# Kernel optimization log

Measured on AMD Instinct MI355X. Metric: run time of the kernel, lower is better.

## Reference

```python
import jax, jax.numpy as jnp
import numpy as np

N_NODES = 10000
N_EDGES = 80000
A, C, D = 2, 15, 64     # batch, temporal dim (15 fixed by fc conv kernel), feature dim
OUT_DIM = 10            # fixed by fc conv kernel width
N_GIN = 2               # num_layers - 1 GIN conv layers
BN_EPS = 1e-5


def bn_last(x, g, b):
    # torch BatchNorm2d (training-mode batch stats) with channels on the LAST axis;
    # original code permutes (0,3,2,1) around BN, which is equivalent to normalizing axis -1.
    m = x.mean(axis=(0, 1, 2), keepdims=True)
    v = x.var(axis=(0, 1, 2), keepdims=True)  # biased var, as torch uses in forward
    return (x - m) * jax.lax.rsqrt(v + BN_EPS) * g + b


def setup_inputs() -> dict:
    key = jax.random.key(0)
    ks = jax.random.split(key, 16)
    s = 0.05
    f32 = jnp.float32
    return {
        "h": jax.random.normal(ks[0], (A, D, C, N_NODES), f32),
        # GIN layer params, stacked over the 2 layers (input_dim == hidden_dim == 64)
        "eps": jnp.zeros((N_GIN,), f32),                                   # learn_eps, init 0
        "W0": (jax.random.normal(ks[1], (N_GIN, D, D), f32) * s),          # MLP linear 0
        "b0": jnp.zeros((N_GIN, D), f32),
        "g0": jnp.ones((N_GIN, D), f32),                                   # MLP BN
        "be0": jnp.zeros((N_GIN, D), f32),
        "W1": (jax.random.normal(ks[2], (N_GIN, D, D), f32) * s),          # MLP linear 1
        "b1": jnp.zeros((N_GIN, D), f32),
        "ga": jnp.ones((N_GIN, D), f32),                                   # ApplyNodeFunc BN
        "ba": jnp.zeros((N_GIN, D), f32),
        "go": jnp.ones((N_GIN, D), f32),                                   # outer GIN BN
        "bo": jnp.zeros((N_GIN, D), f32),
        # per-hidden-rep prediction linears (3 = num_layers)
        "Wp": (jax.random.normal(ks[3], (N_GIN + 1, D, OUT_DIM), f32) * s),
        "bp": jnp.zeros((N_GIN + 1, OUT_DIM), f32),
        # final Conv2d(1,1,(15,10)) == full-extent weighted sum
        "Wfc": (jax.random.normal(ks[4], (C, OUT_DIM), f32) * s),
        "bfc": jnp.zeros((1,), f32),
        # graph edge list (src -> dst aggregation)
        "src": jax.random.randint(ks[5], (N_EDGES,), 0, N_NODES, jnp.int32),
        "dst": jax.random.randint(ks[6], (N_EDGES,), 0, N_NODES, jnp.int32),
    }


def reference(h, eps, W0, b0, g0, be0, W1, b1, ga, ba, go, bo, Wp, bp, Wfc, bfc, src, dst):
    # h: [A, D, C, N] -> node-first layout [N, A, C, D] (the two transposes in torch)
    x = jnp.transpose(h, (3, 0, 2, 1))
    hidden_rep = [x]
    for l in range(N_GIN):
        # GINConv, sum aggregation: (1+eps)*h + sum_{src->dst} h[src]
        agg = jax.ops.segment_sum(x[src], dst, num_segments=N_NODES)
        z = (1.0 + eps[l]) * x + agg
        # MLP (2 layers): linear -> BN -> relu -> linear
        z = jax.nn.relu(bn_last(z @ W0[l] + b0[l], g0[l], be0[l]))
        z = z @ W1[l] + b1[l]
        # ApplyNodeFunc: BN + relu
        z = jax.nn.relu(bn_last(z, ga[l], ba[l]))
        # outer per-layer BN + relu (GIN.forward)
        x = jax.nn.relu(bn_last(z, go[l], bo[l]))
        hidden_rep.append(x)
    # multi-scale readout: sum-pool over nodes, per-layer linear score (dropout is eval/no-op)
    score = jnp.zeros((A, C, OUT_DIM), h.dtype)
    for i, r in enumerate(hidden_rep):
        pooled = r.sum(axis=0)                       # [A, C, D]
        score = score + pooled @ Wp[i] + bp[i]
    # fc: Conv2d(1,1,(15,10)) over [A,1,C,OUT_DIM] then squeeze twice -> [A, 1]
    out = jnp.einsum('ach,ch->a', score, Wfc) + bfc[0]
    return out[:, None]
```

## Files before the change

### kernel.cpp

```cpp
#include <hip/hip_runtime.h>
#include <hip/hip_bf16.h>

#define N_NODES   10000
#define N_EDGES   80000
#define R_TOTAL   300000
#define ELEMS     19200000
#define NODE_F    1920
#define N_TILES   18750
#define PD_GRID   640
#define GEMM_GRID 1024
#define RP_BGRP   16

typedef __attribute__((ext_vector_type(8))) short short8;
typedef __attribute__((ext_vector_type(4))) float f32x4;
typedef __attribute__((ext_vector_type(4))) unsigned int u32x4;
typedef __attribute__((ext_vector_type(2))) unsigned int u32x2;
typedef unsigned short ushort_t;

__device__ __forceinline__ unsigned short f2bf(float f) {
    unsigned u = __builtin_bit_cast(unsigned, f);
    unsigned r = u + 0x7fff + ((u >> 16) & 1);
    return (unsigned short)(r >> 16);
}
__device__ __forceinline__ float lo_f(unsigned u) { return __builtin_bit_cast(float, u << 16); }
__device__ __forceinline__ float hi_f(unsigned u) { return __builtin_bit_cast(float, u & 0xffff0000u); }
__device__ __forceinline__ unsigned packbf(float lo, float hi) {
    return ((unsigned)f2bf(hi) << 16) | (unsigned)f2bf(lo);
}

__device__ __forceinline__ void bn_coef(const float* __restrict__ ssum,
                                        const float* __restrict__ ssq,
                                        const float* __restrict__ g,
                                        const float* __restrict__ b, int j,
                                        float& sc, float& sh) {
    const float invM = 1.0f / (float)R_TOTAL;
    float m = ssum[j] * invM;
    float v = ssq[j] * invM - m * m;
    sc = g[j] * rsqrtf(v + 1e-5f);
    sh = b[j] - m * sc;
}

__global__ __launch_bounds__(256) void k_transpose(const float* __restrict__ h,
                                                   ushort_t* __restrict__ xb,
                                                   float* __restrict__ pooled) {
    __shared__ float tile[64][65];
    int tn = blockIdx.x;
    int ac = blockIdx.y;
    int a = ac / 15, c = ac % 15;
    int t = threadIdx.x;
    int n0 = tn * 64;

    int r = t >> 4, g = t & 15;
    int nbase = n0 + 4 * g;
    const float* hp = h + (size_t)a * 9600000 + (size_t)c * 10000;
#pragma unroll
    for (int it = 0; it < 4; it++) {
        int d = it * 16 + r;
        const float* p = hp + (size_t)d * 150000 + nbase;
        float4 v;
        if (nbase + 3 < N_NODES) {
            v = *(const float4*)p;
        } else {
            v.x = (nbase + 0 < N_NODES) ? p[0] : 0.f;
            v.y = (nbase + 1 < N_NODES) ? p[1] : 0.f;
            v.z = (nbase + 2 < N_NODES) ? p[2] : 0.f;
            v.w = (nbase + 3 < N_NODES) ? p[3] : 0.f;
        }
        tile[d][4 * g + 0] = v.x;
        tile[d][4 * g + 1] = v.y;
        tile[d][4 * g + 2] = v.z;
        tile[d][4 * g + 3] = v.w;
    }
    __syncthreads();

    int nn = t >> 2, dg = (t & 3) * 16;
    int n = n0 + nn;
    if (n < N_NODES) {
        u32x4 oA, oB;
#pragma unroll
        for (int q = 0; q < 4; q++) {
            oA[q] = packbf(tile[dg + 2 * q][nn],     tile[dg + 2 * q + 1][nn]);
            oB[q] = packbf(tile[dg + 8 + 2 * q][nn], tile[dg + 8 + 2 * q + 1][nn]);
        }
        ushort_t* dst = xb + ((size_t)(n * 30 + ac)) * 64 + dg;
        *(u32x4*)dst = oA;
        *(u32x4*)(dst + 8) = oB;
    }

    if (t < 64) {
        float s = 0.f;
        int lim = min(64, N_NODES - n0);
        for (int j = 0; j < lim; j++) s += tile[t][j];
        atomicAdd(&pooled[ac * 64 + t], s);
    }
}

__global__ void k_deg(const int* __restrict__ dst, int* __restrict__ deg) {
    int e = blockIdx.x * 256 + threadIdx.x;
    if (e < N_EDGES) atomicAdd(&deg[dst[e]], 1);
}

__global__ __launch_bounds__(256) void k_scan(const int* __restrict__ deg,
                                              int* __restrict__ off,
                                              int* __restrict__ cursor) {
    __shared__ int buf[256];
    int t = threadIdx.x;
    int c0 = t * 40;
    int local[40];
    int s = 0;
    for (int i = 0; i < 40; i++) {
        int idx = c0 + i;
        int d = (idx < N_NODES) ? deg[idx] : 0;
        local[i] = d;
        s += d;
    }
    buf[t] = s;
    __syncthreads();
    for (int st = 1; st < 256; st <<= 1) {
        int v = (t >= st) ? buf[t - st] : 0;
        __syncthreads();
        buf[t] += v;
        __syncthreads();
    }
    int run = buf[t] - s;
    for (int i = 0; i < 40; i++) {
        int idx = c0 + i;
        if (idx < N_NODES) {
            off[idx] = run;
            cursor[idx] = run;
            run += local[i];
        }
    }
    if (t == 255) off[N_NODES] = buf[255];
}

__global__ void k_fill(const int* __restrict__ src, const int* __restrict__ dst,
                       int* __restrict__ cursor, int* __restrict__ csr) {
    int e = blockIdx.x * 256 + threadIdx.x;
    if (e < N_EDGES) {
        int p = atomicAdd(&cursor[dst[e]], 1);
        csr[p] = src[e];
    }
}

__global__ __launch_bounds__(256) void k_gather(const ushort_t* __restrict__ xb,
                                                ushort_t* __restrict__ aggb,
                                                const int* __restrict__ off,
                                                const int* __restrict__ csr) {
    __shared__ int eds[256];
    int n = blockIdx.x;
    int t = threadIdx.x;
    bool act = t < 240;
    int e0 = off[n], e1 = off[n + 1];
    float acc[8] = {0.f, 0.f, 0.f, 0.f, 0.f, 0.f, 0.f, 0.f};
    for (int base = e0; base < e1; base += 256) {
        int cnt = min(256, e1 - base);
        __syncthreads();
        if (t < cnt) eds[t] = csr[base + t];
        __syncthreads();
        if (act) {
            int i = 0;
            for (; i + 4 <= cnt; i += 4) {
                u32x4 v0 = *(const u32x4*)(xb + (size_t)eds[i + 0] * NODE_F + t * 8);
                u32x4 v1 = *(const u32x4*)(xb + (size_t)eds[i + 1] * NODE_F + t * 8);
                u32x4 v2 = *(const u32x4*)(xb + (size_t)eds[i + 2] * NODE_F + t * 8);
                u32x4 v3 = *(const u32x4*)(xb + (size_t)eds[i + 3] * NODE_F + t * 8);
#pragma unroll
                for (int q = 0; q < 4; q++) {
                    acc[2 * q]     += lo_f(v0[q]) + lo_f(v1[q]) + lo_f(v2[q]) + lo_f(v3[q]);
                    acc[2 * q + 1] += hi_f(v0[q]) + hi_f(v1[q]) + hi_f(v2[q]) + hi_f(v3[q]);
                }
            }
            for (; i < cnt; i++) {
                u32x4 v = *(const u32x4*)(xb + (size_t)eds[i] * NODE_F + t * 8);
#pragma unroll
                for (int q = 0; q < 4; q++) {
                    acc[2 * q]     += lo_f(v[q]);
                    acc[2 * q + 1] += hi_f(v[q]);
                }
            }
        }
    }
    if (act) {
        u32x4 o;
#pragma unroll
        for (int q = 0; q < 4; q++) o[q] = packbf(acc[2 * q], acc[2 * q + 1]);
        *(u32x4*)(aggb + (size_t)n * NODE_F + t * 8) = o;
    }
}

__global__ __launch_bounds__(256) void k_passA(const ushort_t* __restrict__ xb,
                                               const ushort_t* __restrict__ aggb,
                                               ushort_t* __restrict__ to,
                                               const float* __restrict__ W,
                                               const float* __restrict__ bias,
                                               const float* __restrict__ epsp, int l,
                                               float* __restrict__ ssum, float* __restrict__ ssq) {
    int tid = threadIdx.x;
    int lane = tid & 63, wid = tid >> 6;
    int m = lane & 15, kg = lane >> 4;

    short8 bfr[2][4];
#pragma unroll
    for (int s = 0; s < 2; s++)
#pragma unroll
        for (int nt = 0; nt < 4; nt++) {
            short8 v;
#pragma unroll
            for (int j = 0; j < 8; j++)
                v[j] = (short)f2bf(W[(s * 32 + kg * 8 + j) * 64 + 4 * m + nt]);
            bfr[s][nt] = v;
        }
    float bcol[4];
#pragma unroll
    for (int nt = 0; nt < 4; nt++) bcol[nt] = bias[4 * m + nt];
    float e1 = 1.0f + epsp[l];

    float s0a[4] = {0.f, 0.f, 0.f, 0.f}, s1a[4] = {0.f, 0.f, 0.f, 0.f};

    for (int tile = blockIdx.x * 4 + wid; tile < N_TILES; tile += gridDim.x * 4) {
        size_t row0 = (size_t)tile * 16;
        const u32x4* xr = (const u32x4*)(xb + (row0 + m) * 64);
        const u32x4* ar = (const u32x4*)(aggb + (row0 + m) * 64);
        short8 afr[2];
#pragma unroll
        for (int s = 0; s < 2; s++) {
            u32x4 xv = xr[s * 4 + kg];
            u32x4 av = ar[s * 4 + kg];
            u32x4 zv;
#pragma unroll
            for (int q = 0; q < 4; q++) {
                float zl = fmaf(e1, lo_f(xv[q]), lo_f(av[q]));
                float zh = fmaf(e1, hi_f(xv[q]), hi_f(av[q]));
                zv[q] = packbf(zl, zh);
            }
            afr[s] = __builtin_bit_cast(short8, zv);
        }
        f32x4 acc0 = {0,0,0,0}, acc1 = {0,0,0,0}, acc2 = {0,0,0,0}, acc3 = {0,0,0,0};
#pragma unroll
        for (int s = 0; s < 2; s++) {
            acc0 = __builtin_amdgcn_mfma_f32_16x16x32_bf16(afr[s], bfr[s][0], acc0, 0, 0, 0);
            acc1 = __builtin_amdgcn_mfma_f32_16x16x32_bf16(afr[s], bfr[s][1], acc1, 0, 0, 0);
            acc2 = __builtin_amdgcn_mfma_f32_16x16x32_bf16(afr[s], bfr[s][2], acc2, 0, 0, 0);
            acc3 = __builtin_amdgcn_mfma_f32_16x16x32_bf16(afr[s], bfr[s][3], acc3, 0, 0, 0);
        }
        ushort_t* tw = to + (row0 + kg * 4) * 64 + 4 * m;
#pragma unroll
        for (int r = 0; r < 4; r++) {
            float v0 = acc0[r] + bcol[0];
            float v1 = acc1[r] + bcol[1];
            float v2 = acc2[r] + bcol[2];
            float v3 = acc3[r] + bcol[3];
            u32x2 pk;
            pk[0] = packbf(v0, v1);
            pk[1] = packbf(v2, v3);
            *(u32x2*)(tw + (size_t)r * 64) = pk;
            s0a[0] += v0; s1a[0] += v0 * v0;
            s0a[1] += v1; s1a[1] += v1 * v1;
            s0a[2] += v2; s1a[2] += v2 * v2;
            s0a[3] += v3; s1a[3] += v3 * v3;
        }
    }
    __shared__ float shs0[64], shs1[64];
    if (tid < 64) { shs0[tid] = 0.f; shs1[tid] = 0.f; }
    __syncthreads();
#pragma unroll
    for (int nt = 0; nt < 4; nt++) {
        atomicAdd(&shs0[4 * m + nt], s0a[nt]);
        atomicAdd(&shs1[4 * m + nt], s1a[nt]);
    }
    __syncthreads();
    if (tid < 64) {
        atomicAdd(&ssum[tid], shs0[tid]);
        atomicAdd(&ssq[tid], shs1[tid]);
    }
}

__global__ __launch_bounds__(256) void k_passB(const ushort_t* __restrict__ ti,
                                               ushort_t* __restrict__ to,
                                               const float* __restrict__ W,
                                               const float* __restrict__ bias,
                                               const float* __restrict__ ssum0,
                                               const float* __restrict__ ssq0,
                                               const float* __restrict__ g0,
                                               const float* __restrict__ be0,
                                               float* __restrict__ ssum, float* __restrict__ ssq) {
    int tid = threadIdx.x;
    int lane = tid & 63, wid = tid >> 6;
    int m = lane & 15, kg = lane >> 4;

    short8 bfr[2][4];
#pragma unroll
    for (int s = 0; s < 2; s++)
#pragma unroll
        for (int nt = 0; nt < 4; nt++) {
            short8 v;
#pragma unroll
            for (int j = 0; j < 8; j++)
                v[j] = (short)f2bf(W[(s * 32 + kg * 8 + j) * 64 + 4 * m + nt]);
            bfr[s][nt] = v;
        }
    float bcol[4];
#pragma unroll
    for (int nt = 0; nt < 4; nt++) bcol[nt] = bias[4 * m + nt];
    float scv[2][8], shv[2][8];
#pragma unroll
    for (int s = 0; s < 2; s++)
#pragma unroll
        for (int j = 0; j < 8; j++)
            bn_coef(ssum0, ssq0, g0, be0, s * 32 + kg * 8 + j, scv[s][j], shv[s][j]);

    float s0a[4] = {0.f, 0.f, 0.f, 0.f}, s1a[4] = {0.f, 0.f, 0.f, 0.f};

    for (int tile = blockIdx.x * 4 + wid; tile < N_TILES; tile += gridDim.x * 4) {
        size_t row0 = (size_t)tile * 16;
        const u32x4* tr = (const u32x4*)(ti + (row0 + m) * 64);
        short8 afr[2];
#pragma unroll
        for (int s = 0; s < 2; s++) {
            u32x4 tv = tr[s * 4 + kg];
            u32x4 zv;
#pragma unroll
            for (int q = 0; q < 4; q++) {
                float zl = fmaxf(fmaf(lo_f(tv[q]), scv[s][2 * q],     shv[s][2 * q]),     0.f);
                float zh = fmaxf(fmaf(hi_f(tv[q]), scv[s][2 * q + 1], shv[s][2 * q + 1]), 0.f);
                zv[q] = packbf(zl, zh);
            }
            afr[s] = __builtin_bit_cast(short8, zv);
        }
        f32x4 acc0 = {0,0,0,0}, acc1 = {0,0,0,0}, acc2 = {0,0,0,0}, acc3 = {0,0,0,0};
#pragma unroll
        for (int s = 0; s < 2; s++) {
            acc0 = __builtin_amdgcn_mfma_f32_16x16x32_bf16(afr[s], bfr[s][0], acc0, 0, 0, 0);
            acc1 = __builtin_amdgcn_mfma_f32_16x16x32_bf16(afr[s], bfr[s][1], acc1, 0, 0, 0);
            acc2 = __builtin_amdgcn_mfma_f32_16x16x32_bf16(afr[s], bfr[s][2], acc2, 0, 0, 0);
            acc3 = __builtin_amdgcn_mfma_f32_16x16x32_bf16(afr[s], bfr[s][3], acc3, 0, 0, 0);
        }
        ushort_t* tw = to + (row0 + kg * 4) * 64 + 4 * m;
#pragma unroll
        for (int r = 0; r < 4; r++) {
            float v0 = acc0[r] + bcol[0];
            float v1 = acc1[r] + bcol[1];
            float v2 = acc2[r] + bcol[2];
            float v3 = acc3[r] + bcol[3];
            u32x2 pk;
            pk[0] = packbf(v0, v1);
            pk[1] = packbf(v2, v3);
            *(u32x2*)(tw + (size_t)r * 64) = pk;
            s0a[0] += v0; s1a[0] += v0 * v0;
            s0a[1] += v1; s1a[1] += v1 * v1;
            s0a[2] += v2; s1a[2] += v2 * v2;
            s0a[3] += v3; s1a[3] += v3 * v3;
        }
    }
    __shared__ float shs0[64], shs1[64];
    if (tid < 64) { shs0[tid] = 0.f; shs1[tid] = 0.f; }
    __syncthreads();
#pragma unroll
    for (int nt = 0; nt < 4; nt++) {
        atomicAdd(&shs0[4 * m + nt], s0a[nt]);
        atomicAdd(&shs1[4 * m + nt], s1a[nt]);
    }
    __syncthreads();
    if (tid < 64) {
        atomicAdd(&ssum[tid], shs0[tid]);
        atomicAdd(&ssq[tid], shs1[tid]);
    }
}

__global__ __launch_bounds__(256) void k_statsC(const ushort_t* __restrict__ tb,
                                                const float* __restrict__ ssum1,
                                                const float* __restrict__ ssq1,
                                                const float* __restrict__ ga,
                                                const float* __restrict__ ba,
                                                float* __restrict__ ssum2,
                                                float* __restrict__ ssq2) {
    __shared__ float shs0[64], shs1[64];
    int tid = threadIdx.x;
    if (tid < 64) { shs0[tid] = 0.f; shs1[tid] = 0.f; }
    __syncthreads();
    int ch0 = (tid & 7) * 8;
    float sc[8], sh[8];
#pragma unroll
    for (int j = 0; j < 8; j++) bn_coef(ssum1, ssq1, ga, ba, ch0 + j, sc[j], sh[j]);
    float s0[8] = {0,0,0,0,0,0,0,0}, s1[8] = {0,0,0,0,0,0,0,0};
    const u32x4* t4 = (const u32x4*)tb;
    const int total = ELEMS / 8;
    int stride = gridDim.x * 256;
    for (int i = blockIdx.x * 256 + tid; i < total; i += stride) {
        u32x4 v = t4[i];
#pragma unroll
        for (int q = 0; q < 4; q++) {
            float e;
            e = fmaxf(fmaf(lo_f(v[q]), sc[2 * q],     sh[2 * q]),     0.f);
            s0[2 * q] += e;     s1[2 * q] += e * e;
            e = fmaxf(fmaf(hi_f(v[q]), sc[2 * q + 1], sh[2 * q + 1]), 0.f);
            s0[2 * q + 1] += e; s1[2 * q + 1] += e * e;
        }
    }
#pragma unroll
    for (int j = 0; j < 8; j++) {
        atomicAdd(&shs0[ch0 + j], s0[j]);
        atomicAdd(&shs1[ch0 + j], s1[j]);
    }
    __syncthreads();
    if (tid < 64) {
        atomicAdd(&ssum2[tid], shs0[tid]);
        atomicAdd(&ssq2[tid], shs1[tid]);
    }
}

__global__ __launch_bounds__(256) void k_passD(const ushort_t* __restrict__ tb,
                                               ushort_t* __restrict__ xb,
                                               const float* __restrict__ ssum1,
                                               const float* __restrict__ ssq1,
                                               const float* __restrict__ ga,
                                               const float* __restrict__ ba,
                                               const float* __restrict__ ssum2,
                                               const float* __restrict__ ssq2,
                                               const float* __restrict__ go,
                                               const float* __restrict__ bo,
                                               float* __restrict__ pp,
                                               int writeX) {
    int t = threadIdx.x;
    bool act = t < 240;
    int ch0 = (t & 7) * 8;
    float sc1[8], sh1[8], sc2[8], sh2[8];
#pragma unroll
    for (int j = 0; j < 8; j++) {
        bn_coef(ssum1, ssq1, ga, ba, ch0 + j, sc1[j], sh1[j]);
        bn_coef(ssum2, ssq2, go, bo, ch0 + j, sc2[j], sh2[j]);
    }
    float pool[8] = {0,0,0,0,0,0,0,0};
    if (act) {
        for (int n = blockIdx.x; n < N_NODES; n += gridDim.x) {
            const u32x4* tr = (const u32x4*)(tb + (size_t)n * NODE_F);
            u32x4 v = tr[t];
            u32x4 o;
#pragma unroll
            for (int q = 0; q < 4; q++) {
                float el = fmaxf(fmaf(fmaxf(fmaf(lo_f(v[q]), sc1[2 * q], sh1[2 * q]), 0.f),
                                      sc2[2 * q], sh2[2 * q]), 0.f);
                float eh = fmaxf(fmaf(fmaxf(fmaf(hi_f(v[q]), sc1[2 * q + 1], sh1[2 * q + 1]), 0.f),
                                      sc2[2 * q + 1], sh2[2 * q + 1]), 0.f);
                pool[2 * q] += el;
                pool[2 * q + 1] += eh;
                o[q] = packbf(el, eh);
            }
            if (writeX) *(u32x4*)(xb + (size_t)n * NODE_F + t * 8) = o;
        }
        float4* pb = (float4*)(pp + (size_t)blockIdx.x * NODE_F + t * 8);
        pb[0] = make_float4(pool[0], pool[1], pool[2], pool[3]);
        pb[1] = make_float4(pool[4], pool[5], pool[6], pool[7]);
    }
}

__global__ __launch_bounds__(256) void k_redpool(const float* __restrict__ pp,
                                                 float* __restrict__ pooled) {
    int ch = blockIdx.x * 256 + threadIdx.x;
    if (ch >= NODE_F) return;
    const int per = PD_GRID / RP_BGRP;
    int b0 = blockIdx.y * per;
    float a0 = 0.f, a1 = 0.f, a2 = 0.f, a3 = 0.f;
    for (int b = b0; b < b0 + per; b += 4) {
        a0 += pp[(size_t)(b + 0) * NODE_F + ch];
        a1 += pp[(size_t)(b + 1) * NODE_F + ch];
        a2 += pp[(size_t)(b + 2) * NODE_F + ch];
        a3 += pp[(size_t)(b + 3) * NODE_F + ch];
    }
    atomicAdd(&pooled[ch], (a0 + a1) + (a2 + a3));
}

__global__ void k_final(const float* __restrict__ pooled,
                        const float* __restrict__ Wp,
                        const float* __restrict__ bp,
                        const float* __restrict__ Wfc,
                        const float* __restrict__ bfc, float* __restrict__ out) {
    __shared__ float oa[2];
    int t = threadIdx.x;
    if (t < 2) oa[t] = 0.f;
    __syncthreads();
    if (t < 300) {
        int a = t / 150, rem = t % 150, c = rem / 10, hh = rem % 10;
        int ac = a * 15 + c;
        float sc_sum = 0.f;
        for (int i = 0; i < 3; i++) {
            float s = bp[i * 10 + hh];
            const float* pp = pooled + i * NODE_F + ac * 64;
            const float* wp = Wp + i * 640 + hh;
            for (int d = 0; d < 64; d++) s += pp[d] * wp[d * 10];
            sc_sum += s;
        }
        atomicAdd(&oa[a], sc_sum * Wfc[c * 10 + hh]);
    }
    __syncthreads();
    if (t < 2) out[t] = oa[t] + bfc[0];
}

extern "C" void kernel_launch(void* const* d_in, const int* in_sizes, int n_in,
                              void* d_out, int out_size, void* d_ws, size_t ws_size,
                              hipStream_t stream) {
    const float* h   = (const float*)d_in[0];
    const float* eps = (const float*)d_in[1];
    const float* W0  = (const float*)d_in[2];
    const float* b0  = (const float*)d_in[3];
    const float* g0  = (const float*)d_in[4];
    const float* be0 = (const float*)d_in[5];
    const float* W1  = (const float*)d_in[6];
    const float* b1  = (const float*)d_in[7];
    const float* ga  = (const float*)d_in[8];
    const float* ba  = (const float*)d_in[9];
    const float* go  = (const float*)d_in[10];
    const float* bo  = (const float*)d_in[11];
    const float* Wp  = (const float*)d_in[12];
    const float* bp  = (const float*)d_in[13];
    const float* Wfc = (const float*)d_in[14];
    const float* bfc = (const float*)d_in[15];
    const int*   src = (const int*)d_in[16];
    const int*   dst = (const int*)d_in[17];
    float* out = (float*)d_out;

    ushort_t* xb   = (ushort_t*)d_ws;
    ushort_t* bufP = xb + ELEMS;
    ushort_t* bufQ = bufP + ELEMS;
    float* small   = (float*)(bufQ + ELEMS);
    float* bn = small;
    float* pooled = small + 6 * 256;
    int* ideg = (int*)(pooled + 3 * NODE_F);
    int* ioff = ideg + N_NODES;
    int* icur = ioff + N_NODES + 1;
    int* icsr = icur + N_NODES;
    float* pp0 = (float*)(icsr + N_EDGES);
    float* pp1 = pp0 + (size_t)PD_GRID * NODE_F;

    hipMemsetAsync(small, 0,
                   (6 * 256 + 3 * NODE_F) * sizeof(float) + N_NODES * sizeof(int), stream);

    k_deg<<<(N_EDGES + 255) / 256, 256, 0, stream>>>(dst, ideg);
    k_scan<<<1, 256, 0, stream>>>(ideg, ioff, icur);
    k_fill<<<(N_EDGES + 255) / 256, 256, 0, stream>>>(src, dst, icur, icsr);

    k_transpose<<<dim3(157, 30), 256, 0, stream>>>(h, xb, pooled);

    for (int l = 0; l < 2; l++) {
        float* s0s = bn + l * 3 * 256;
        float* s1s = s0s + 256;
        float* s2s = s1s + 256;
        float* ppl = (l == 0) ? pp0 : pp1;
        k_gather<<<N_NODES, 256, 0, stream>>>(xb, bufP, ioff, icsr);
        k_passA<<<GEMM_GRID, 256, 0, stream>>>(xb, bufP, bufQ,
                                               W0 + l * 4096, b0 + l * 64, eps, l,
                                               s0s, s0s + 64);
        k_passB<<<GEMM_GRID, 256, 0, stream>>>(bufQ, bufP, W1 + l * 4096, b1 + l * 64,
                                               s0s, s0s + 64, g0 + l * 64, be0 + l * 64,
                                               s1s, s1s + 64);
        k_statsC<<<1024, 256, 0, stream>>>(bufP, s1s, s1s + 64, ga + l * 64, ba + l * 64,
                                           s2s, s2s + 64);
        k_passD<<<PD_GRID, 256, 0, stream>>>(bufP, xb, s1s, s1s + 64, ga + l * 64, ba + l * 64,
                                             s2s, s2s + 64, go + l * 64, bo + l * 64,
                                             ppl, (l == 0) ? 1 : 0);
    }
    k_redpool<<<dim3(8, RP_BGRP), 256, 0, stream>>>(pp0, pooled + 1 * NODE_F);
    k_redpool<<<dim3(8, RP_BGRP), 256, 0, stream>>>(pp1, pooled + 2 * NODE_F);
    k_final<<<1, 320, 0, stream>>>(pooled, Wp, bp, Wfc, bfc, out);
}
```

Baseline: 453.6 us.

## Fuse neighbor gather with first MLP linear and merge redpool launches

Combines the edge-sum gather and the first GEMM (with the (1+eps)*x term and BN stat accumulation) into one kernel. Each block aggregates two nodes into shared memory, then runs MFMA on the resulting 60 rows padded to 64. The bf16 aggregate buffer no longer has to be written and read back through global memory, and one launch is saved per layer. In exchange, every block reconverts the weights and the GEMM work is spread thinly over 5000 blocks. The two pooling-reduction launches are also merged into a single launch using a z grid dimension.

```diff
diff --git a/kernel.cpp b/kernel.cpp
--- a/kernel.cpp
+++ b/kernel.cpp
@@ -143,136 +143,151 @@
     }
 }
 
-__global__ __launch_bounds__(256) void k_gather(const ushort_t* __restrict__ xb,
-                                                ushort_t* __restrict__ aggb,
-                                                const int* __restrict__ off,
-                                                const int* __restrict__ csr) {
-    __shared__ int eds[256];
-    int n = blockIdx.x;
+__global__ __launch_bounds__(256) void k_gmlp(const ushort_t* __restrict__ xb,
+                                              ushort_t* __restrict__ to,
+                                              const int* __restrict__ off,
+                                              const int* __restrict__ csr,
+                                              const float* __restrict__ W,
+                                              const float* __restrict__ bias,
+                                              const float* __restrict__ epsp, int l,
+                                              float* __restrict__ ssum,
+                                              float* __restrict__ ssq) {
+    __shared__ ushort_t zl[64][72];
+    __shared__ ushort_t wl[64][72];
+    __shared__ int eds[64];
+    __shared__ float shs0[64], shs1[64];
+
     int t = threadIdx.x;
+    int lane = t & 63, w = t >> 6;
+    int m = lane & 15, kg = lane >> 4;
+
+    {
+        const float4* W4 = (const float4*)W;
+#pragma unroll
+        for (int it = 0; it < 4; it++) {
+            int e = it * 1024 + t * 4;
+            float4 v = W4[e >> 2];
+            int k = e >> 6, col = e & 63;
+            wl[col + 0][k] = f2bf(v.x);
+            wl[col + 1][k] = f2bf(v.y);
+            wl[col + 2][k] = f2bf(v.z);
+            wl[col + 3][k] = f2bf(v.w);
+        }
+    }
+    if (t < 64) { shs0[t] = 0.f; shs1[t] = 0.f; }
+    if (t >= 224) {
+        int tt = t - 224;
+        int row = (tt >> 3) < 2 ? 30 + (tt >> 3) : 60 + (tt >> 3);
+        *(u32x4*)&zl[row][(tt & 7) * 8] = (u32x4){0, 0, 0, 0};
+    }
+
+    float e1 = 1.0f + epsp[l];
+    int n0 = blockIdx.x * 2;
     bool act = t < 240;
-    int e0 = off[n], e1 = off[n + 1];
-    float acc[8] = {0.f, 0.f, 0.f, 0.f, 0.f, 0.f, 0.f, 0.f};
-    for (int base = e0; base < e1; base += 256) {
-        int cnt = min(256, e1 - base);
-        __syncthreads();
-        if (t < cnt) eds[t] = csr[base + t];
-        __syncthreads();
+    int r = t >> 3, c8 = (t & 7) * 8;
+
+    for (int ni = 0; ni < 2; ni++) {
+        int n = n0 + ni;
+        float acc[8];
         if (act) {
-            int i = 0;
-            for (; i + 4 <= cnt; i += 4) {
-                u32x4 v0 = *(const u32x4*)(xb + (size_t)eds[i + 0] * NODE_F + t * 8);
-                u32x4 v1 = *(const u32x4*)(xb + (size_t)eds[i + 1] * NODE_F + t * 8);
-                u32x4 v2 = *(const u32x4*)(xb + (size_t)eds[i + 2] * NODE_F + t * 8);
-                u32x4 v3 = *(const u32x4*)(xb + (size_t)eds[i + 3] * NODE_F + t * 8);
-#pragma unroll
-                for (int q = 0; q < 4; q++) {
-                    acc[2 * q]     += lo_f(v0[q]) + lo_f(v1[q]) + lo_f(v2[q]) + lo_f(v3[q]);
-                    acc[2 * q + 1] += hi_f(v0[q]) + hi_f(v1[q]) + hi_f(v2[q]) + hi_f(v3[q]);
+            u32x4 xv = *(const u32x4*)(xb + (size_t)n * NODE_F + t * 8);
+#pragma unroll
+            for (int q = 0; q < 4; q++) {
+                acc[2 * q]     = e1 * lo_f(xv[q]);
+                acc[2 * q + 1] = e1 * hi_f(xv[q]);
+            }
+        }
+        int e0 = off[n], eE = off[n + 1];
+        for (int base = e0; base < eE; base += 64) {
+            int cnt = min(64, eE - base);
+            __syncthreads();
+            if (t < cnt) eds[t] = csr[base + t];
+            __syncthreads();
+            if (act) {
+                int i = 0;
+                for (; i + 4 <= cnt; i += 4) {
+                    u32x4 v0 = *(const u32x4*)(xb + (size_t)eds[i + 0] * NODE_F + t * 8);
+                    u32x4 v1 = *(const u32x4*)(xb + (size_t)eds[i + 1] * NODE_F + t * 8);
+                    u32x4 v2 = *(const u32x4*)(xb + (size_t)eds[i + 2] * NODE_F + t * 8);
+                    u32x4 v3 = *(const u32x4*)(xb + (size_t)eds[i + 3] * NODE_F + t * 8);
+#pragma unroll
+                    for (int q = 0; q < 4; q++) {
+                        acc[2 * q]     += lo_f(v0[q]) + lo_f(v1[q]) + lo_f(v2[q]) + lo_f(v3[q]);
+                        acc[2 * q + 1] += hi_f(v0[q]) + hi_f(v1[q]) + hi_f(v2[q]) + hi_f(v3[q]);
+                    }
+                }
+                for (; i < cnt; i++) {
+                    u32x4 v = *(const u32x4*)(xb + (size_t)eds[i] * NODE_F + t * 8);
+#pragma unroll
+                    for (int q = 0; q < 4; q++) {
+                        acc[2 * q]     += lo_f(v[q]);
+                        acc[2 * q + 1] += hi_f(v[q]);
+                    }
                 }
             }
-            for (; i < cnt; i++) {
-                u32x4 v = *(const u32x4*)(xb + (size_t)eds[i] * NODE_F + t * 8);
-#pragma unroll
-                for (int q = 0; q < 4; q++) {
-                    acc[2 * q]     += lo_f(v[q]);
-                    acc[2 * q + 1] += hi_f(v[q]);
-                }
-            }
-        }
-    }
-    if (act) {
-        u32x4 o;
-#pragma unroll
-        for (int q = 0; q < 4; q++) o[q] = packbf(acc[2 * q], acc[2 * q + 1]);
-        *(u32x4*)(aggb + (size_t)n * NODE_F + t * 8) = o;
-    }
-}
-
-__global__ __launch_bounds__(256) void k_passA(const ushort_t* __restrict__ xb,
-                                               const ushort_t* __restrict__ aggb,
-                                               ushort_t* __restrict__ to,
-                                               const float* __restrict__ W,
-                                               const float* __restrict__ bias,
-                                               const float* __restrict__ epsp, int l,
-                                               float* __restrict__ ssum, float* __restrict__ ssq) {
-    int tid = threadIdx.x;
-    int lane = tid & 63, wid = tid >> 6;
-    int m = lane & 15, kg = lane >> 4;
+        }
+        if (act) {
+            u32x4 o;
+#pragma unroll
+            for (int q = 0; q < 4; q++) o[q] = packbf(acc[2 * q], acc[2 * q + 1]);
+            *(u32x4*)&zl[ni * 32 + r][c8] = o;
+        }
+    }
+    __syncthreads();
 
     short8 bfr[2][4];
 #pragma unroll
     for (int s = 0; s < 2; s++)
 #pragma unroll
-        for (int nt = 0; nt < 4; nt++) {
-            short8 v;
-#pragma unroll
-            for (int j = 0; j < 8; j++)
-                v[j] = (short)f2bf(W[(s * 32 + kg * 8 + j) * 64 + 4 * m + nt]);
-            bfr[s][nt] = v;
-        }
+        for (int nt = 0; nt < 4; nt++)
+            bfr[s][nt] = *(const short8*)&wl[4 * m + nt][s * 32 + kg * 8];
+    short8 afr[2];
+#pragma unroll
+    for (int s = 0; s < 2; s++)
+        afr[s] = *(const short8*)&zl[w * 16 + m][s * 32 + kg * 8];
+
+    f32x4 acc0 = {0,0,0,0}, acc1 = {0,0,0,0}, acc2 = {0,0,0,0}, acc3 = {0,0,0,0};
+#pragma unroll
+    for (int s = 0; s < 2; s++) {
+        acc0 = __builtin_amdgcn_mfma_f32_16x16x32_bf16(afr[s], bfr[s][0], acc0, 0, 0, 0);
+        acc1 = __builtin_amdgcn_mfma_f32_16x16x32_bf16(afr[s], bfr[s][1], acc1, 0, 0, 0);
+        acc2 = __builtin_amdgcn_mfma_f32_16x16x32_bf16(afr[s], bfr[s][2], acc2, 0, 0, 0);
+        acc3 = __builtin_amdgcn_mfma_f32_16x16x32_bf16(afr[s], bfr[s][3], acc3, 0, 0, 0);
+    }
     float bcol[4];
 #pragma unroll
     for (int nt = 0; nt < 4; nt++) bcol[nt] = bias[4 * m + nt];
-    float e1 = 1.0f + epsp[l];
 
     float s0a[4] = {0.f, 0.f, 0.f, 0.f}, s1a[4] = {0.f, 0.f, 0.f, 0.f};
-
-    for (int tile = blockIdx.x * 4 + wid; tile < N_TILES; tile += gridDim.x * 4) {
-        size_t row0 = (size_t)tile * 16;
-        const u32x4* xr = (const u32x4*)(xb + (row0 + m) * 64);
-        const u32x4* ar = (const u32x4*)(aggb + (row0 + m) * 64);
-        short8 afr[2];
-#pragma unroll
-        for (int s = 0; s < 2; s++) {
-            u32x4 xv = xr[s * 4 + kg];
-            u32x4 av = ar[s * 4 + kg];
-            u32x4 zv;
-#pragma unroll
-            for (int q = 0; q < 4; q++) {
-                float zl = fmaf(e1, lo_f(xv[q]), lo_f(av[q]));
-                float zh = fmaf(e1, hi_f(xv[q]), hi_f(av[q]));
-                zv[q] = packbf(zl, zh);
-            }
-            afr[s] = __builtin_bit_cast(short8, zv);
-        }
-        f32x4 acc0 = {0,0,0,0}, acc1 = {0,0,0,0}, acc2 = {0,0,0,0}, acc3 = {0,0,0,0};
-#pragma unroll
-        for (int s = 0; s < 2; s++) {
-            acc0 = __builtin_amdgcn_mfma_f32_16x16x32_bf16(afr[s], bfr[s][0], acc0, 0, 0, 0);
-            acc1 = __builtin_amdgcn_mfma_f32_16x16x32_bf16(afr[s], bfr[s][1], acc1, 0, 0, 0);
-            acc2 = __builtin_amdgcn_mfma_f32_16x16x32_bf16(afr[s], bfr[s][2], acc2, 0, 0, 0);
-            acc3 = __builtin_amdgcn_mfma_f32_16x16x32_bf16(afr[s], bfr[s][3], acc3, 0, 0, 0);
-        }
-        ushort_t* tw = to + (row0 + kg * 4) * 64 + 4 * m;
-#pragma unroll
-        for (int r = 0; r < 4; r++) {
-            float v0 = acc0[r] + bcol[0];
-            float v1 = acc1[r] + bcol[1];
-            float v2 = acc2[r] + bcol[2];
-            float v3 = acc3[r] + bcol[3];
+    int node = n0 + (w >> 1);
+    int lrbase = (w & 1) * 16 + kg * 4;
+#pragma unroll
+    for (int rr = 0; rr < 4; rr++) {
+        int lr = lrbase + rr;
+        if (lr < 30) {
+            float v0 = acc0[rr] + bcol[0];
+            float v1 = acc1[rr] + bcol[1];
+            float v2 = acc2[rr] + bcol[2];
+            float v3 = acc3[rr] + bcol[3];
             u32x2 pk;
             pk[0] = packbf(v0, v1);
             pk[1] = packbf(v2, v3);
-            *(u32x2*)(tw + (size_t)r * 64) = pk;
+            *(u32x2*)(to + ((size_t)node * 30 + lr) * 64 + 4 * m) = pk;
             s0a[0] += v0; s1a[0] += v0 * v0;
             s0a[1] += v1; s1a[1] += v1 * v1;
             s0a[2] += v2; s1a[2] += v2 * v2;
             s0a[3] += v3; s1a[3] += v3 * v3;
         }
     }
-    __shared__ float shs0[64], shs1[64];
-    if (tid < 64) { shs0[tid] = 0.f; shs1[tid] = 0.f; }
-    __syncthreads();
 #pragma unroll
     for (int nt = 0; nt < 4; nt++) {
         atomicAdd(&shs0[4 * m + nt], s0a[nt]);
         atomicAdd(&shs1[4 * m + nt], s1a[nt]);
     }
     __syncthreads();
-    if (tid < 64) {
-        atomicAdd(&ssum[tid], shs0[tid]);
-        atomicAdd(&ssq[tid], shs1[tid]);
+    if (t < 64) {
+        atomicAdd(&ssum[t], shs0[t]);
+        atomicAdd(&ssq[t], shs1[t]);
     }
 }
 
@@ -322,9 +337,9 @@
             u32x4 zv;
 #pragma unroll
             for (int q = 0; q < 4; q++) {
-                float zl = fmaxf(fmaf(lo_f(tv[q]), scv[s][2 * q],     shv[s][2 * q]),     0.f);
-                float zh = fmaxf(fmaf(hi_f(tv[q]), scv[s][2 * q + 1], shv[s][2 * q + 1]), 0.f);
-                zv[q] = packbf(zl, zh);
+                float zl_ = fmaxf(fmaf(lo_f(tv[q]), scv[s][2 * q],     shv[s][2 * q]),     0.f);
+                float zh_ = fmaxf(fmaf(hi_f(tv[q]), scv[s][2 * q + 1], shv[s][2 * q + 1]), 0.f);
+                zv[q] = packbf(zl_, zh_);
             }
             afr[s] = __builtin_bit_cast(short8, zv);
         }
@@ -455,10 +470,13 @@
     }
 }
 
-__global__ __launch_bounds__(256) void k_redpool(const float* __restrict__ pp,
+__global__ __launch_bounds__(256) void k_redpool(const float* __restrict__ pp0,
+                                                 const float* __restrict__ pp1,
                                                  float* __restrict__ pooled) {
     int ch = blockIdx.x * 256 + threadIdx.x;
     if (ch >= NODE_F) return;
+    const float* pp = (blockIdx.z == 0) ? pp0 : pp1;
+    float* dstp = pooled + (blockIdx.z + 1) * NODE_F;
     const int per = PD_GRID / RP_BGRP;
     int b0 = blockIdx.y * per;
     float a0 = 0.f, a1 = 0.f, a2 = 0.f, a3 = 0.f;
@@ -468,7 +486,7 @@
         a2 += pp[(size_t)(b + 2) * NODE_F + ch];
         a3 += pp[(size_t)(b + 3) * NODE_F + ch];
     }
-    atomicAdd(&pooled[ch], (a0 + a1) + (a2 + a3));
+    atomicAdd(&dstp[ch], (a0 + a1) + (a2 + a3));
 }
 
 __global__ void k_final(const float* __restrict__ pooled,
@@ -547,10 +565,9 @@
         float* s1s = s0s + 256;
         float* s2s = s1s + 256;
         float* ppl = (l == 0) ? pp0 : pp1;
-        k_gather<<<N_NODES, 256, 0, stream>>>(xb, bufP, ioff, icsr);
-        k_passA<<<GEMM_GRID, 256, 0, stream>>>(xb, bufP, bufQ,
-                                               W0 + l * 4096, b0 + l * 64, eps, l,
-                                               s0s, s0s + 64);
+        k_gmlp<<<N_NODES / 2, 256, 0, stream>>>(xb, bufQ, ioff, icsr,
+                                                W0 + l * 4096, b0 + l * 64, eps, l,
+                                                s0s, s0s + 64);
         k_passB<<<GEMM_GRID, 256, 0, stream>>>(bufQ, bufP, W1 + l * 4096, b1 + l * 64,
                                                s0s, s0s + 64, g0 + l * 64, be0 + l * 64,
                                                s1s, s1s + 64);
@@ -560,7 +577,6 @@
                                              s2s, s2s + 64, go + l * 64, bo + l * 64,
                                              ppl, (l == 0) ? 1 : 0);
     }
-    k_redpool<<<dim3(8, RP_BGRP), 256, 0, stream>>>(pp0, pooled + 1 * NODE_F);
-    k_redpool<<<dim3(8, RP_BGRP), 256, 0, stream>>>(pp1, pooled + 2 * NODE_F);
+    k_redpool<<<dim3(8, RP_BGRP, 2), 256, 0, stream>>>(pp0, pp1, pooled);
     k_final<<<1, 320, 0, stream>>>(pooled, Wp, bp, Wfc, bfc, out);
 }
```

New measurement: 561.5 us. 1.24x slower.

## Switch node features to slice-major layout with XCD-aware gather partitioning

Applied to the files above, without the earlier changes.

Node features are now stored as [A*C][N][64] instead of [N][A*C][64]. The gather kernel gives each (a,c) slice to a fixed XCD group, so each slice's 1.28MB working set can stay in one XCD's L2 while 8 threads per node read 128-byte rows. passD and the pooling reduction are restructured around the new layout, with pooling partial sums reduced in LDS and a smaller per-slice partial buffer. The XCD mapping assumes round-robin block dispatch across 8 XCDs, and passA/passB treat rows generically, so they stay correct.

```diff
diff --git a/kernel.cpp b/kernel.cpp
--- a/kernel.cpp
+++ b/kernel.cpp
@@ -7,9 +7,9 @@
 #define ELEMS     19200000
 #define NODE_F    1920
 #define N_TILES   18750
-#define PD_GRID   640
 #define GEMM_GRID 1024
-#define RP_BGRP   16
+#define BPS       313
+#define PD_X      40
 
 typedef __attribute__((ext_vector_type(8))) short short8;
 typedef __attribute__((ext_vector_type(4))) float f32x4;
@@ -82,7 +82,7 @@
             oA[q] = packbf(tile[dg + 2 * q][nn],     tile[dg + 2 * q + 1][nn]);
             oB[q] = packbf(tile[dg + 8 + 2 * q][nn], tile[dg + 8 + 2 * q + 1][nn]);
         }
-        ushort_t* dst = xb + ((size_t)(n * 30 + ac)) * 64 + dg;
+        ushort_t* dst = xb + ((size_t)ac * N_NODES + n) * 64 + dg;
         *(u32x4*)dst = oA;
         *(u32x4*)(dst + 8) = oB;
     }
@@ -143,50 +143,52 @@
     }
 }
 
-__global__ __launch_bounds__(256) void k_gather(const ushort_t* __restrict__ xb,
-                                                ushort_t* __restrict__ aggb,
+__global__ __launch_bounds__(256) void k_gather(const ushort_t* __restrict__ xs,
+                                                ushort_t* __restrict__ aggs,
                                                 const int* __restrict__ off,
                                                 const int* __restrict__ csr) {
-    __shared__ int eds[256];
-    int n = blockIdx.x;
+    int bid = blockIdx.x;
+    int xcd = bid & 7, k = bid >> 3;
+    int base = (xcd < 6) ? xcd * 4 : 24 + (xcd - 6) * 3;
+    int nsl  = (xcd < 6) ? 4 : 3;
+    int si = k / BPS;
+    if (si >= nsl) return;
+    int ac = base + si;
+    int ng = k - si * BPS;
     int t = threadIdx.x;
-    bool act = t < 240;
+    int nl = t >> 3, c8 = t & 7;
+    int n = ng * 32 + nl;
+    if (n >= N_NODES) return;
+
+    const ushort_t* xsl = xs + (size_t)ac * N_NODES * 64;
+    float acc[8] = {0.f, 0.f, 0.f, 0.f, 0.f, 0.f, 0.f, 0.f};
     int e0 = off[n], e1 = off[n + 1];
-    float acc[8] = {0.f, 0.f, 0.f, 0.f, 0.f, 0.f, 0.f, 0.f};
-    for (int base = e0; base < e1; base += 256) {
-        int cnt = min(256, e1 - base);
-        __syncthreads();
-        if (t < cnt) eds[t] = csr[base + t];
-        __syncthreads();
-        if (act) {
-            int i = 0;
-            for (; i + 4 <= cnt; i += 4) {
-                u32x4 v0 = *(const u32x4*)(xb + (size_t)eds[i + 0] * NODE_F + t * 8);
-                u32x4 v1 = *(const u32x4*)(xb + (size_t)eds[i + 1] * NODE_F + t * 8);
-                u32x4 v2 = *(const u32x4*)(xb + (size_t)eds[i + 2] * NODE_F + t * 8);
-                u32x4 v3 = *(const u32x4*)(xb + (size_t)eds[i + 3] * NODE_F + t * 8);
-#pragma unroll
-                for (int q = 0; q < 4; q++) {
-                    acc[2 * q]     += lo_f(v0[q]) + lo_f(v1[q]) + lo_f(v2[q]) + lo_f(v3[q]);
-                    acc[2 * q + 1] += hi_f(v0[q]) + hi_f(v1[q]) + hi_f(v2[q]) + hi_f(v3[q]);
-                }
-            }
-            for (; i < cnt; i++) {
-                u32x4 v = *(const u32x4*)(xb + (size_t)eds[i] * NODE_F + t * 8);
-#pragma unroll
-                for (int q = 0; q < 4; q++) {
-                    acc[2 * q]     += lo_f(v[q]);
-                    acc[2 * q + 1] += hi_f(v[q]);
-                }
-            }
-        }
-    }
-    if (act) {
-        u32x4 o;
-#pragma unroll
-        for (int q = 0; q < 4; q++) o[q] = packbf(acc[2 * q], acc[2 * q + 1]);
-        *(u32x4*)(aggb + (size_t)n * NODE_F + t * 8) = o;
-    }
+    int i = e0;
+    for (; i + 4 <= e1; i += 4) {
+        int s0 = csr[i], s1 = csr[i + 1], s2 = csr[i + 2], s3 = csr[i + 3];
+        u32x4 v0 = *(const u32x4*)(xsl + (size_t)s0 * 64 + c8 * 8);
+        u32x4 v1 = *(const u32x4*)(xsl + (size_t)s1 * 64 + c8 * 8);
+        u32x4 v2 = *(const u32x4*)(xsl + (size_t)s2 * 64 + c8 * 8);
+        u32x4 v3 = *(const u32x4*)(xsl + (size_t)s3 * 64 + c8 * 8);
+#pragma unroll
+        for (int q = 0; q < 4; q++) {
+            acc[2 * q]     += (lo_f(v0[q]) + lo_f(v1[q])) + (lo_f(v2[q]) + lo_f(v3[q]));
+            acc[2 * q + 1] += (hi_f(v0[q]) + hi_f(v1[q])) + (hi_f(v2[q]) + hi_f(v3[q]));
+        }
+    }
+    for (; i < e1; i++) {
+        int s0 = csr[i];
+        u32x4 v = *(const u32x4*)(xsl + (size_t)s0 * 64 + c8 * 8);
+#pragma unroll
+        for (int q = 0; q < 4; q++) {
+            acc[2 * q]     += lo_f(v[q]);
+            acc[2 * q + 1] += hi_f(v[q]);
+        }
+    }
+    u32x4 o;
+#pragma unroll
+    for (int q = 0; q < 4; q++) o[q] = packbf(acc[2 * q], acc[2 * q + 1]);
+    *(u32x4*)(aggs + ((size_t)ac * N_NODES + n) * 64 + c8 * 8) = o;
 }
 
 __global__ __launch_bounds__(256) void k_passA(const ushort_t* __restrict__ xb,
@@ -322,9 +324,9 @@
             u32x4 zv;
 #pragma unroll
             for (int q = 0; q < 4; q++) {
-                float zl = fmaxf(fmaf(lo_f(tv[q]), scv[s][2 * q],     shv[s][2 * q]),     0.f);
-                float zh = fmaxf(fmaf(hi_f(tv[q]), scv[s][2 * q + 1], shv[s][2 * q + 1]), 0.f);
-                zv[q] = packbf(zl, zh);
+                float zl_ = fmaxf(fmaf(lo_f(tv[q]), scv[s][2 * q],     shv[s][2 * q]),     0.f);
+                float zh_ = fmaxf(fmaf(hi_f(tv[q]), scv[s][2 * q + 1], shv[s][2 * q + 1]), 0.f);
+                zv[q] = packbf(zl_, zh_);
             }
             afr[s] = __builtin_bit_cast(short8, zv);
         }
@@ -422,53 +424,54 @@
                                                const float* __restrict__ bo,
                                                float* __restrict__ pp,
                                                int writeX) {
+    __shared__ float pl[64];
     int t = threadIdx.x;
-    bool act = t < 240;
-    int ch0 = (t & 7) * 8;
+    int nl = t >> 3, c8 = t & 7;
+    int ac = blockIdx.y, bx = blockIdx.x;
+    int ch0 = c8 * 8;
     float sc1[8], sh1[8], sc2[8], sh2[8];
 #pragma unroll
     for (int j = 0; j < 8; j++) {
         bn_coef(ssum1, ssq1, ga, ba, ch0 + j, sc1[j], sh1[j]);
         bn_coef(ssum2, ssq2, go, bo, ch0 + j, sc2[j], sh2[j]);
     }
+    if (t < 64) pl[t] = 0.f;
+    __syncthreads();
+
     float pool[8] = {0,0,0,0,0,0,0,0};
-    if (act) {
-        for (int n = blockIdx.x; n < N_NODES; n += gridDim.x) {
-            const u32x4* tr = (const u32x4*)(tb + (size_t)n * NODE_F);
-            u32x4 v = tr[t];
-            u32x4 o;
-#pragma unroll
-            for (int q = 0; q < 4; q++) {
-                float el = fmaxf(fmaf(fmaxf(fmaf(lo_f(v[q]), sc1[2 * q], sh1[2 * q]), 0.f),
-                                      sc2[2 * q], sh2[2 * q]), 0.f);
-                float eh = fmaxf(fmaf(fmaxf(fmaf(hi_f(v[q]), sc1[2 * q + 1], sh1[2 * q + 1]), 0.f),
-                                      sc2[2 * q + 1], sh2[2 * q + 1]), 0.f);
-                pool[2 * q] += el;
-                pool[2 * q + 1] += eh;
-                o[q] = packbf(el, eh);
-            }
-            if (writeX) *(u32x4*)(xb + (size_t)n * NODE_F + t * 8) = o;
-        }
-        float4* pb = (float4*)(pp + (size_t)blockIdx.x * NODE_F + t * 8);
-        pb[0] = make_float4(pool[0], pool[1], pool[2], pool[3]);
-        pb[1] = make_float4(pool[4], pool[5], pool[6], pool[7]);
-    }
-}
-
-__global__ __launch_bounds__(256) void k_redpool(const float* __restrict__ pp,
+    int n0 = bx * 250;
+    for (int n = n0 + nl; n < n0 + 250; n += 32) {
+        size_t r = (size_t)ac * N_NODES + n;
+        u32x4 v = *(const u32x4*)(tb + r * 64 + ch0);
+        u32x4 o;
+#pragma unroll
+        for (int q = 0; q < 4; q++) {
+            float el = fmaxf(fmaf(fmaxf(fmaf(lo_f(v[q]), sc1[2 * q], sh1[2 * q]), 0.f),
+                                  sc2[2 * q], sh2[2 * q]), 0.f);
+            float eh = fmaxf(fmaf(fmaxf(fmaf(hi_f(v[q]), sc1[2 * q + 1], sh1[2 * q + 1]), 0.f),
+                                  sc2[2 * q + 1], sh2[2 * q + 1]), 0.f);
+            pool[2 * q] += el;
+            pool[2 * q + 1] += eh;
+            o[q] = packbf(el, eh);
+        }
+        if (writeX) *(u32x4*)(xb + r * 64 + ch0) = o;
+    }
+#pragma unroll
+    for (int j = 0; j < 8; j++) atomicAdd(&pl[ch0 + j], pool[j]);
+    __syncthreads();
+    if (t < 64) pp[((size_t)ac * PD_X + bx) * 64 + t] = pl[t];
+}
+
+__global__ __launch_bounds__(256) void k_redpool(const float* __restrict__ pp0,
+                                                 const float* __restrict__ pp1,
                                                  float* __restrict__ pooled) {
     int ch = blockIdx.x * 256 + threadIdx.x;
     if (ch >= NODE_F) return;
-    const int per = PD_GRID / RP_BGRP;
-    int b0 = blockIdx.y * per;
-    float a0 = 0.f, a1 = 0.f, a2 = 0.f, a3 = 0.f;
-    for (int b = b0; b < b0 + per; b += 4) {
-        a0 += pp[(size_t)(b + 0) * NODE_F + ch];
-        a1 += pp[(size_t)(b + 1) * NODE_F + ch];
-        a2 += pp[(size_t)(b + 2) * NODE_F + ch];
-        a3 += pp[(size_t)(b + 3) * NODE_F + ch];
-    }
-    atomicAdd(&pooled[ch], (a0 + a1) + (a2 + a3));
+    const float* pp = (blockIdx.z == 0) ? pp0 : pp1;
+    int ac = ch >> 6, d = ch & 63;
+    float a = 0.f;
+    for (int b = 0; b < PD_X; b++) a += pp[((size_t)ac * PD_X + b) * 64 + d];
+    pooled[(blockIdx.z + 1) * NODE_F + ch] = a;
 }
 
 __global__ void k_final(const float* __restrict__ pooled,
@@ -531,7 +534,7 @@
     int* icur = ioff + N_NODES + 1;
     int* icsr = icur + N_NODES;
     float* pp0 = (float*)(icsr + N_EDGES);
-    float* pp1 = pp0 + (size_t)PD_GRID * NODE_F;
+    float* pp1 = pp0 + 30 * PD_X * 64;
 
     hipMemsetAsync(small, 0,
                    (6 * 256 + 3 * NODE_F) * sizeof(float) + N_NODES * sizeof(int), stream);
@@ -547,7 +550,7 @@
         float* s1s = s0s + 256;
         float* s2s = s1s + 256;
         float* ppl = (l == 0) ? pp0 : pp1;
-        k_gather<<<N_NODES, 256, 0, stream>>>(xb, bufP, ioff, icsr);
+        k_gather<<<8 * 4 * BPS, 256, 0, stream>>>(xb, bufP, ioff, icsr);
         k_passA<<<GEMM_GRID, 256, 0, stream>>>(xb, bufP, bufQ,
                                                W0 + l * 4096, b0 + l * 64, eps, l,
                                                s0s, s0s + 64);
@@ -556,11 +559,11 @@
                                                s1s, s1s + 64);
         k_statsC<<<1024, 256, 0, stream>>>(bufP, s1s, s1s + 64, ga + l * 64, ba + l * 64,
                                            s2s, s2s + 64);
-        k_passD<<<PD_GRID, 256, 0, stream>>>(bufP, xb, s1s, s1s + 64, ga + l * 64, ba + l * 64,
-                                             s2s, s2s + 64, go + l * 64, bo + l * 64,
-                                             ppl, (l == 0) ? 1 : 0);
-    }
-    k_redpool<<<dim3(8, RP_BGRP), 256, 0, stream>>>(pp0, pooled + 1 * NODE_F);
-    k_redpool<<<dim3(8, RP_BGRP), 256, 0, stream>>>(pp1, pooled + 2 * NODE_F);
+        k_passD<<<dim3(PD_X, 30), 256, 0, stream>>>(bufP, xb, s1s, s1s + 64,
+                                                    ga + l * 64, ba + l * 64,
+                                                    s2s, s2s + 64, go + l * 64, bo + l * 64,
+                                                    ppl, (l == 0) ? 1 : 0);
+    }
+    k_redpool<<<dim3(8, 1, 2), 256, 0, stream>>>(pp0, pp1, pooled);
     k_final<<<1, 320, 0, stream>>>(pooled, Wp, bp, Wfc, bfc, out);
 }
```

Result: faster. 432.4 us (-4.7%).
